# Kernel tuning notes

Measured on AMD Instinct MI355X. Metric: run time of the kernel, lower is better.

The kernel has to match this reference:

```python
import jax, jax.numpy as jnp
import numpy as np

B, N, H, MEM, V = 512, 50, 256, 8, 40001
SCALE = 1.0 / float(np.sqrt(H))
NEG = -1e12


def sinusoid_table(n_pos, d):
    pos = np.arange(n_pos)[:, None].astype(np.float64)
    j = np.arange(d)[None, :]
    ang = pos / np.power(10000.0, 2 * (j // 2) / d)
    tab = np.zeros((n_pos, d))
    tab[:, 0::2] = np.sin(ang[:, 0::2])
    tab[:, 1::2] = np.cos(ang[:, 1::2])
    return jnp.asarray(tab, jnp.float32)

TAB = sinusoid_table(N, H)


def setup_inputs():
    key = jax.random.key(0)
    ks = jax.random.split(key, 40)
    s = 0.05
    rn = lambda k, shp, sc=s: jax.random.normal(k, shp, jnp.float32) * sc
    lengths = jax.random.randint(ks[0], (B,), 1, N + 1)
    mask = (jnp.arange(N)[None, :] < lengths[:, None]).astype(jnp.int32)
    item_flag = jax.random.randint(ks[1], (B, V - 1), 0, 2).astype(jnp.int32)
    inp = {
        'seq_emb_1': rn(ks[2], (B, N, H), 1.0),
        'seq_emb_2': rn(ks[3], (B, N, H), 1.0),
        'mask': mask,
        'item_flag': item_flag,
        # 2-layer GRU (torch layout: W_ih [3H,H], W_hh [3H,H])
        'gru_wih0': rn(ks[4], (3 * H, H)), 'gru_whh0': rn(ks[5], (3 * H, H)),
        'gru_bih0': rn(ks[6], (3 * H,)), 'gru_bhh0': rn(ks[7], (3 * H,)),
        'gru_wih1': rn(ks[8], (3 * H, H)), 'gru_whh1': rn(ks[9], (3 * H, H)),
        'gru_bih1': rn(ks[10], (3 * H,)), 'gru_bhh1': rn(ks[11], (3 * H,)),
        # attention projections ([in,out] layout, y = x @ W)
        'Wq1': rn(ks[12], (H, H)), 'Wk1': rn(ks[13], (H, H)), 'Wv1': rn(ks[14], (H, H)),
        'Wq2': rn(ks[15], (H, H)), 'Wk2': rn(ks[16], (H, H)), 'Wv2': rn(ks[17], (H, H)),
        'W_ffn1': rn(ks[18], (H, H)), 'b_ffn1': rn(ks[19], (H,)),
        'W_ffn2': rn(ks[20], (H, H)), 'b_ffn2': rn(ks[21], (H,)),
        'W_one1': rn(ks[22], (H, H)), 'b_one1': rn(ks[23], (H,)),
        'W_three1': rn(ks[24], (2 * H, 1)),
        'W_trans1': rn(ks[25], (2 * H, H)), 'b_trans1': rn(ks[26], (H,)),
        'W_tail1': rn(ks[27], (H, H)), 'b_tail1': rn(ks[28], (H,)),
        'W_tail2': rn(ks[29], (H, 2)),
        'mem_k': rn(ks[30], (1, MEM, H)), 'mem_v': rn(ks[31], (1, MEM, H)),
        'emb1': rn(ks[32], (V, H)),
    }
    return inp


def _gru_layer(x, wih, whh, bih, bhh):
    # x: [B,N,H] -> [B,N,H], h0 = 0 (torch default)
    def step(h, xt):
        gi = xt @ wih.T + bih
        gh = h @ whh.T + bhh
        ir, iz, inn = jnp.split(gi, 3, axis=-1)
        hr, hz, hn = jnp.split(gh, 3, axis=-1)
        r = jax.nn.sigmoid(ir + hr)
        z = jax.nn.sigmoid(iz + hz)
        n = jnp.tanh(inn + r * hn)
        h2 = (1.0 - z) * n + z * h
        return h2, h2
    h0 = jnp.zeros((x.shape[0], H), x.dtype)
    _, ys = jax.lax.scan(step, h0, jnp.swapaxes(x, 0, 1))
    return jnp.swapaxes(ys, 0, 1)


def _co_attention(q, k, v, mask, mem_k=None, mem_v=None):
    b = q.shape[0]
    causal = jnp.tril(jnp.ones((N, N), bool))           # [N,N]
    pad = mask.astype(bool)[:, None, :]                  # [B,1,N]
    allow_seq = causal[None, :, :] & pad                 # [B,N,N]
    if mem_k is not None:
        k = jnp.concatenate([jnp.broadcast_to(mem_k, (b, MEM, H)), k], axis=1)
        v = jnp.concatenate([jnp.broadcast_to(mem_v, (b, MEM, H)), v], axis=1)
        mem_ok = jnp.ones((b, N, MEM), bool)             # memory keys always visible
        allow = jnp.concatenate([mem_ok, allow_seq], axis=-1)
    else:
        allow = allow_seq
    att = jnp.einsum('bqh,bkh->bqk', q, k) * SCALE
    att = jax.nn.softmax(jnp.where(allow, att, NEG), axis=-1)
    return jnp.einsum('bqk,bkh->bqh', att, v) * mask[:, :, None].astype(q.dtype)


def reference(seq_emb_1, seq_emb_2, mask, item_flag,
              gru_wih0, gru_whh0, gru_bih0, gru_bhh0,
              gru_wih1, gru_whh1, gru_bih1, gru_bhh1,
              Wq1, Wk1, Wv1, Wq2, Wk2, Wv2,
              W_ffn1, b_ffn1, W_ffn2, b_ffn2,
              W_one1, b_one1, W_three1, W_trans1, b_trans1,
              W_tail1, b_tail1, W_tail2, mem_k, mem_v, emb1):
    b = mask.shape[0]
    mf = mask[:, :, None].astype(jnp.float32)
    # 2-layer GRU on stream 2
    s2 = _gru_layer(seq_emb_2, gru_wih0, gru_whh0, gru_bih0, gru_bhh0)
    s2 = _gru_layer(s2, gru_wih1, gru_whh1, gru_bih1, gru_bhh1)
    last = jnp.sum(mask, axis=1) - 1                     # last valid index
    sr_l_1 = seq_emb_1[jnp.arange(b), last]              # [B,H]
    q1_1 = sr_l_1 @ W_one1 + b_one1 + TAB[0]
    se1 = seq_emb_1 * mf
    # positional encoding indexed by |pos - last_idx|
    flag = jnp.abs(jnp.arange(N, dtype=jnp.int32)[None, :] - last[:, None].astype(jnp.int32))
    pe = TAB[flag]                                       # [B,N,H]
    q1 = se1 @ Wq1 + pe
    k1 = se1 @ Wk1 + pe
    v1 = se1 @ Wv1 + pe
    att1 = _co_attention(q1, k1, v1, mask) @ W_ffn1 + b_ffn1
    se2 = s2 * mf
    k2 = se2 @ Wk2
    v2 = se2 @ Wv2
    att2 = _co_attention(q1, k2, v2, mask, mem_k, mem_v) @ W_ffn2 + b_ffn2
    att = jax.nn.relu(att1 + att2)
    alpha = jnp.concatenate([att, jnp.broadcast_to(q1_1[:, None, :], att.shape)], axis=-1) @ W_three1
    alpha = jax.nn.softmax(jnp.where(mf > 0, alpha, NEG), axis=1)  # [B,N,1]
    sess = jnp.sum(alpha * se1 * mf, axis=1)
    sess = jnp.concatenate([sess, sr_l_1], axis=1) @ W_trans1 + b_trans1
    item_emb = emb1[1:]                                  # [V-1,H]
    score = sess @ item_emb.T                            # [B,V-1]
    fl = item_flag.astype(bool)
    score_in = jax.nn.softmax(jnp.where(fl, score, NEG), axis=-1)
    score_ex = jax.nn.softmax(jnp.where(fl, NEG, score), axis=-1)
    beta = jax.nn.softmax(jax.nn.relu(sess @ W_tail1 + b_tail1) @ W_tail2, axis=-1)  # [B,2]
    boundary = jnp.mean(jnp.abs(beta[:, 0] - beta[:, 1]))
    final = score_in * beta[:, 0:1] + score_ex * beta[:, 1:2]
    return final[:, None, :], boundary
```

## Files before the change

kernel.cpp:

```cpp
#include <hip/hip_runtime.h>
#include <hip/hip_bf16.h>
#include <cstdint>
#include <cstddef>

#define Bsz 512
#define Nsq 50
#define Hd  256
#define VM1 40000
static constexpr float SCALE_C = 0.0625f;
static constexpr float NEG_C   = -1.0e12f;

typedef __attribute__((ext_vector_type(8))) short bf16x8;
typedef __attribute__((ext_vector_type(4))) float f32x4;

__device__ __forceinline__ float sigmoidf_(float x) { return 1.0f / (1.0f + __expf(-x)); }
__device__ __forceinline__ float tanh_fast(float x) {
  float t = fminf(fmaxf(2.0f * x, -60.0f), 60.0f);
  float e = __expf(t);
  return (e - 1.0f) / (e + 1.0f);
}
__device__ __forceinline__ ushort f2b(float x) {
  union { float f; uint32_t u; } c; c.f = x;
  uint32_t r = (c.u + 0x7fffu + ((c.u >> 16) & 1u)) >> 16;
  return (ushort)r;
}
__device__ __forceinline__ uint pk2f(float a, float b) {
  return (uint)f2b(a) | ((uint)f2b(b) << 16);
}
__device__ __forceinline__ uint addpe2(uint w, float pa, float pb) {
  union { float f; uint32_t u; } lo, hi;
  lo.u = (w & 0xffffu) << 16; hi.u = w & 0xffff0000u;
  return pk2f(lo.f + pa, hi.f + pb);
}

__global__ void build_tab(float* __restrict__ TAB) {
  int idx = blockIdx.x * 256 + threadIdx.x;
  int pos = idx >> 8, j = idx & 255;
  int pair = j >> 1;
  float expo = (2.0f * (float)pair) / 256.0f;
  float inv = powf(10000.0f, -expo);
  float ang = (float)pos * inv;
  TAB[idx] = (j & 1) ? cosf(ang) : sinf(ang);
}

__global__ __launch_bounds__(256) void last_srl_kernel(const int* __restrict__ mask,
    const float* __restrict__ seq1, int* __restrict__ lastp, float* __restrict__ srl) {
  int b = blockIdx.x, tid = threadIdx.x;
  __shared__ int ls;
  if (tid == 0) {
    int c = 0;
    for (int t = 0; t < Nsq; ++t) c += mask[b * Nsq + t];
    ls = c - 1;
    lastp[b] = c - 1;
  }
  __syncthreads();
  srl[b * Hd + tid] = seq1[((size_t)b * Nsq + ls) * Hd + tid];
}

template <int BT, int BIAS>
__global__ __launch_bounds__(256) void gemm_tile(const float* __restrict__ A,
    const float* __restrict__ B, const float* __restrict__ bias,
    float* __restrict__ C, int M, int N, int K) {
  __shared__ float As[16][132];
  __shared__ float Bs[16][68];
  int bm = blockIdx.y * 128, bn = blockIdx.x * 64;
  int tid = threadIdx.x;
  int tm = (tid >> 4) << 3;
  int tn = (tid & 15) << 2;
  float acc[8][4] = {};
  for (int k0 = 0; k0 < K; k0 += 16) {
#pragma unroll
    for (int u = 0; u < 8; ++u) {
      int i = tid + u * 256;
      int kk = i & 15, m = i >> 4;
      As[kk][m] = A[(size_t)(bm + m) * K + (k0 + kk)];
    }
#pragma unroll
    for (int u = 0; u < 4; ++u) {
      int i = tid + u * 256;
      if (BT) {
        int kk = i & 15, n = i >> 4;
        Bs[kk][n] = B[(size_t)(bn + n) * K + (k0 + kk)];
      } else {
        int n = i & 63, kk = i >> 6;
        Bs[kk][n] = B[(size_t)(k0 + kk) * N + (bn + n)];
      }
    }
    __syncthreads();
#pragma unroll
    for (int kk = 0; kk < 16; ++kk) {
      float a[8], bb[4];
#pragma unroll
      for (int r = 0; r < 8; ++r) a[r] = As[kk][tm + r];
#pragma unroll
      for (int c = 0; c < 4; ++c) bb[c] = Bs[kk][tn + c];
#pragma unroll
      for (int r = 0; r < 8; ++r)
#pragma unroll
        for (int c = 0; c < 4; ++c) acc[r][c] += a[r] * bb[c];
    }
    __syncthreads();
  }
#pragma unroll
  for (int r = 0; r < 8; ++r) {
    size_t row = (size_t)(bm + tm + r) * N + bn;
#pragma unroll
    for (int c = 0; c < 4; ++c) {
      float v = acc[r][c];
      if (BIAS) v += bias[bn + tn + c];
      C[row + tn + c] = v;
    }
  }
}

template <int BT, int BIAS, int OUTBF>
__global__ __launch_bounds__(256) void mfma_gemm(const ushort* __restrict__ A,
    const ushort* __restrict__ B, const float* __restrict__ bias,
    void* __restrict__ Cv, int M, int N, int K) {
  __shared__ ushort Asm[128 * 32];
  __shared__ ushort Bsm[128 * 40];
  constexpr int SB = BT ? 32 : 40;
  int tid = threadIdx.x;
  int bm = blockIdx.y * 128, bn = blockIdx.x * 128;
  int lane = tid & 63, wave = tid >> 6;
  int quad = lane >> 4, l16 = lane & 15;
  int wm = (wave >> 1) * 64, wn = (wave & 1) * 64;

  int chn0 = wave * 2, chn1 = wave * 2 + 1;
  int ra0 = chn0 * 16 + (lane >> 2), ra1 = chn1 * 16 + (lane >> 2);
  int kc = (lane & 3) * 8;
  const ushort* srcA0 = A + (size_t)(bm + ra0) * K + kc;
  const ushort* srcA1 = A + (size_t)(bm + ra1) * K + kc;
  char* dstA0 = (char*)Asm + chn0 * 1024;
  char* dstA1 = (char*)Asm + chn1 * 1024;
  const ushort* srcB0 = nullptr;
  const ushort* srcB1 = nullptr;
  if (BT) {
    int rb0 = bn + ra0; if (rb0 > N - 1) rb0 = N - 1;
    int rb1 = bn + ra1; if (rb1 > N - 1) rb1 = N - 1;
    srcB0 = B + (size_t)rb0 * K + kc;
    srcB1 = B + (size_t)rb1 * K + kc;
  }
  char* dstB0 = (char*)Bsm + chn0 * 1024;
  char* dstB1 = (char*)Bsm + chn1 * 1024;

  f32x4 acc[4][4] = {};
  for (int k0 = 0; k0 < K; k0 += 32) {
    __builtin_amdgcn_global_load_lds(
        (const __attribute__((address_space(1))) void*)(srcA0 + k0),
        (__attribute__((address_space(3))) void*)dstA0, 16, 0, 0);
    __builtin_amdgcn_global_load_lds(
        (const __attribute__((address_space(1))) void*)(srcA1 + k0),
        (__attribute__((address_space(3))) void*)dstA1, 16, 0, 0);
    if (BT) {
      __builtin_amdgcn_global_load_lds(
          (const __attribute__((address_space(1))) void*)(srcB0 + k0),
          (__attribute__((address_space(3))) void*)dstB0, 16, 0, 0);
      __builtin_amdgcn_global_load_lds(
          (const __attribute__((address_space(1))) void*)(srcB1 + k0),
          (__attribute__((address_space(3))) void*)dstB1, 16, 0, 0);
    } else {
#pragma unroll
      for (int u = 0; u < 8; ++u) {
        int idx = tid + u * 256;
        int n2 = (idx & 63) * 2, kk = idx >> 6;
        uint v = *(const uint*)(B + (size_t)(k0 + kk) * N + bn + n2);
        Bsm[n2 * 40 + kk] = (ushort)(v & 0xffffu);
        Bsm[(n2 + 1) * 40 + kk] = (ushort)(v >> 16);
      }
    }
    __syncthreads();
    bf16x8 af[4], bfr[4];
#pragma unroll
    for (int f = 0; f < 4; ++f) af[f] = *(const bf16x8*)(Asm + (wm + f * 16 + l16) * 32 + quad * 8);
#pragma unroll
    for (int f = 0; f < 4; ++f) bfr[f] = *(const bf16x8*)(Bsm + (wn + f * 16 + l16) * SB + quad * 8);
#pragma unroll
    for (int mf = 0; mf < 4; ++mf)
#pragma unroll
      for (int nf = 0; nf < 4; ++nf)
        acc[mf][nf] = __builtin_amdgcn_mfma_f32_16x16x32_bf16(af[mf], bfr[nf], acc[mf][nf], 0, 0, 0);
    __syncthreads();
  }
#pragma unroll
  for (int mf = 0; mf < 4; ++mf) {
#pragma unroll
    for (int r = 0; r < 4; ++r) {
      int row = bm + wm + mf * 16 + quad * 4 + r;
      size_t rowo = (size_t)row * N;
#pragma unroll
      for (int nf = 0; nf < 4; ++nf) {
        int col = bn + wn + nf * 16 + l16;
        if (col < N) {
          float v = acc[mf][nf][r];
          if (BIAS) v += bias[col];
          if (OUTBF) ((ushort*)Cv)[rowo + col] = f2b(v);
          else       ((float*)Cv)[rowo + col] = v;
        }
      }
    }
  }
}

__global__ void cast_f2b_k(const float* __restrict__ s, ushort* __restrict__ d, int n4) {
  int i = blockIdx.x * 256 + threadIdx.x;
  if (i >= n4) return;
  const float4 v = ((const float4*)s)[i];
  ushort4 o; o.x = f2b(v.x); o.y = f2b(v.y); o.z = f2b(v.z); o.w = f2b(v.w);
  ((ushort4*)d)[i] = o;
}

struct Cast7 { const float* s[7]; ushort* d[7]; };
__global__ void cast7_k(Cast7 p) {
  int m = blockIdx.y;
  int i = blockIdx.x * 256 + threadIdx.x;
  const float4 v = ((const float4*)p.s[m])[i];
  ushort4 o; o.x = f2b(v.x); o.y = f2b(v.y); o.z = f2b(v.z); o.w = f2b(v.w);
  ((ushort4*)p.d[m])[i] = o;
}

__global__ void add_tab0(float* __restrict__ q) {
  int idx = blockIdx.x * 256 + threadIdx.x;
  q[idx] += (float)(threadIdx.x & 1);
}

__global__ void mask_cast(const float* __restrict__ x, const int* __restrict__ m,
                          ushort* __restrict__ yb) {
  int idx = blockIdx.x * 256 + threadIdx.x;
  float v = m[idx >> 8] ? x[idx] : 0.0f;
  yb[idx] = f2b(v);
}

__global__ __launch_bounds__(512, 2) void gru_mfma8_kernel(const float* __restrict__ gi,
    const ushort* __restrict__ whhb, const float* __restrict__ bhh,
    ushort* __restrict__ ysb, const int* __restrict__ mask) {
  __shared__ ushort hbf[2][16][264];
  __shared__ float  gsc[8][2][3][32];
  int tid = threadIdx.x;
  int lane = tid & 63, wave = tid >> 6;
  int quad = lane >> 4, l16 = lane & 15;
  int s0 = blockIdx.x * 2;

  for (int i = tid; i < 2 * 16 * 264 / 2; i += 512) ((uint*)hbf)[i] = 0u;

  bf16x8 bw[48];
#pragma unroll
  for (int f = 0; f < 48; ++f) {
    int nf = f >> 3, kf = f & 7;
    int row = (nf >> 1) * 256 + wave * 32 + (nf & 1) * 16 + l16;
    bw[f] = *(const bf16x8*)(whhb + (size_t)row * 256 + kf * 32 + quad * 8);
  }

  int s = lane >> 5, dloc = lane & 31;
  int d = wave * 32 + dloc;
  float bh0 = bhh[d], bh1 = bhh[256 + d], bh2 = bhh[512 + d];
  const float* gib = gi + (size_t)(s0 + s) * Nsq * 768 + d;
  float g0 = gib[0], g1 = gib[256], g2 = gib[512];
  float hreg = 0.0f;
  const int* mrow = mask + (s0 + s) * Nsq;
  ushort* yrow = ysb + ((size_t)(s0 + s) * Nsq) * 256 + d;
  __syncthreads();

  int cur = 0;
  for (int t = 0; t < Nsq; ++t) {
    int tn = (t + 1 < Nsq) ? t + 1 : t;
    float p0 = gib[tn * 768], p1 = gib[tn * 768 + 256], p2 = gib[tn * 768 + 512];

    f32x4 acc[6] = {};
#pragma unroll
    for (int kf = 0; kf < 8; ++kf) {
      bf16x8 a = *(const bf16x8*)&hbf[cur][l16][kf * 32 + quad * 8];
#pragma unroll
      for (int nf = 0; nf < 6; ++nf)
        acc[nf] = __builtin_amdgcn_mfma_f32_16x16x32_bf16(a, bw[nf * 8 + kf], acc[nf], 0, 0, 0);
    }
    if (quad == 0) {
#pragma unroll
      for (int g = 0; g < 3; ++g)
#pragma unroll
        for (int j = 0; j < 2; ++j) {
          gsc[wave][0][g][j * 16 + l16] = acc[g * 2 + j][0];
          gsc[wave][1][g][j * 16 + l16] = acc[g * 2 + j][1];
        }
    }
    __builtin_amdgcn_sched_barrier(0);

    {
      float ghr = gsc[wave][s][0][dloc];
      float ghz = gsc[wave][s][1][dloc];
      float ghn = gsc[wave][s][2][dloc];
      float rr = sigmoidf_(g0 + ghr + bh0);
      float zz = sigmoidf_(g1 + ghz + bh1);
      float nn = tanh_fast(g2 + rr * (ghn + bh2));
      float h2 = (1.0f - zz) * nn + zz * hreg;
      hreg = h2;
      hbf[cur ^ 1][s][d] = f2b(h2);
      float ov = h2;
      if (mask) ov = mrow[t] ? h2 : 0.0f;
      yrow[t * 256] = f2b(ov);
    }
    g0 = p0; g1 = p1; g2 = p2;
    cur ^= 1;
    __syncthreads();
  }
}

template <int NMEM, int PEQ, int PEKV>
__global__ __launch_bounds__(256) void attn_mfma(const ushort* __restrict__ q1,
    const ushort* __restrict__ kseq, const ushort* __restrict__ vseq,
    const float* __restrict__ kmem, const float* __restrict__ vmem,
    const int* __restrict__ mask, ushort* __restrict__ out,
    const float* __restrict__ TAB, const int* __restrict__ lastp) {
  constexpr int NK = NMEM + Nsq;
  __shared__ ushort KV[64][264];
  __shared__ float Ss[64][66];
  __shared__ ushort Ps[64][72];
  __shared__ int msk[64];
  int tid = threadIdx.x;
  int lane = tid & 63, wave = tid >> 6;
  int quad = lane >> 4, l16 = lane & 15;
  int b = blockIdx.x;
  int last = lastp[b];

  if (tid < 64) msk[tid] = (tid < Nsq) ? mask[b * Nsq + tid] : 0;

#pragma unroll
  for (int it = 0; it < 8; ++it) {
    int idx = tid + it * 256;
    int r = idx >> 5, c8 = (idx & 31) * 8;
    uint4 o4 = make_uint4(0u, 0u, 0u, 0u);
    if (r < Nsq) {
      uint4 v = *(const uint4*)(q1 + (size_t)(b * Nsq + r) * 256 + c8);
      if (PEQ) {
        const float* pe = TAB + abs(r - last) * 256 + c8;
        float4 pa = *(const float4*)pe;
        float4 pb = *(const float4*)(pe + 4);
        o4.x = addpe2(v.x, pa.x, pa.y);
        o4.y = addpe2(v.y, pa.z, pa.w);
        o4.z = addpe2(v.z, pb.x, pb.y);
        o4.w = addpe2(v.w, pb.z, pb.w);
      } else {
        o4 = v;
      }
    }
    *(uint4*)&KV[r][c8] = o4;
  }
  __syncthreads();
  bf16x8 qa[8];
#pragma unroll
  for (int kf = 0; kf < 8; ++kf)
    qa[kf] = *(const bf16x8*)&KV[wave * 16 + l16][kf * 32 + quad * 8];
  __syncthreads();

#pragma unroll
  for (int it = 0; it < 8; ++it) {
    int idx = tid + it * 256;
    int r = idx >> 5, c8 = (idx & 31) * 8;
    uint4 o4 = make_uint4(0u, 0u, 0u, 0u);
    if (r < NK) {
      if (NMEM > 0 && r < NMEM) {
        const float* src = kmem + (size_t)r * 256 + c8;
        float4 a = *(const float4*)src;
        float4 c = *(const float4*)(src + 4);
        o4.x = pk2f(a.x, a.y); o4.y = pk2f(a.z, a.w);
        o4.z = pk2f(c.x, c.y); o4.w = pk2f(c.z, c.w);
      } else {
        uint4 v = *(const uint4*)(kseq + (size_t)(b * Nsq + (r - NMEM)) * 256 + c8);
        if (PEKV) {
          const float* pe = TAB + abs((r - NMEM) - last) * 256 + c8;
          float4 pa = *(const float4*)pe;
          float4 pb = *(const float4*)(pe + 4);
          o4.x = addpe2(v.x, pa.x, pa.y);
          o4.y = addpe2(v.y, pa.z, pa.w);
          o4.z = addpe2(v.z, pb.x, pb.y);
          o4.w = addpe2(v.w, pb.z, pb.w);
        } else {
          o4 = v;
        }
      }
    }
    *(uint4*)&KV[r][c8] = o4;
  }
  __syncthreads();

  {
    f32x4 acc[4] = {};
#pragma unroll
    for (int kf = 0; kf < 8; ++kf) {
#pragma unroll
      for (int nf = 0; nf < 4; ++nf) {
        bf16x8 bf = *(const bf16x8*)&KV[nf * 16 + l16][kf * 32 + quad * 8];
        acc[nf] = __builtin_amdgcn_mfma_f32_16x16x32_bf16(qa[kf], bf, acc[nf], 0, 0, 0);
      }
    }
#pragma unroll
    for (int nf = 0; nf < 4; ++nf)
#pragma unroll
      for (int r = 0; r < 4; ++r)
        Ss[wave * 16 + quad * 4 + r][nf * 16 + l16] = acc[nf][r];
  }
  __syncthreads();

#pragma unroll
  for (int it = 0; it < 8; ++it) {
    int idx = tid + it * 256;
    int r = idx >> 5, c8 = (idx & 31) * 8;
    uint4 o4 = make_uint4(0u, 0u, 0u, 0u);
    if (r < NK) {
      if (NMEM > 0 && r < NMEM) {
        const float* src = vmem + (size_t)r * 256 + c8;
        float4 a = *(const float4*)src;
        float4 c = *(const float4*)(src + 4);
        o4.x = pk2f(a.x, a.y); o4.y = pk2f(a.z, a.w);
        o4.z = pk2f(c.x, c.y); o4.w = pk2f(c.z, c.w);
      } else {
        uint4 v = *(const uint4*)(vseq + (size_t)(b * Nsq + (r - NMEM)) * 256 + c8);
        if (PEKV) {
          const float* pe = TAB + abs((r - NMEM) - last) * 256 + c8;
          float4 pa = *(const float4*)pe;
          float4 pb = *(const float4*)(pe + 4);
          o4.x = addpe2(v.x, pa.x, pa.y);
          o4.y = addpe2(v.y, pa.z, pa.w);
          o4.z = addpe2(v.z, pb.x, pb.y);
          o4.w = addpe2(v.w, pb.z, pb.w);
        } else {
          o4 = v;
        }
      }
    }
    *(uint4*)&KV[r][c8] = o4;
  }
  if (tid < 64) {
    int t = tid;
    if (t < Nsq) {
      float m = -1e30f;
      for (int j = 0; j < NK; ++j) {
        bool ok = (j < NMEM) || (((j - NMEM) <= t) && (msk[j - NMEM] != 0));
        if (ok) m = fmaxf(m, Ss[t][j] * SCALE_C);
      }
      float sum = 0.0f;
      for (int j = 0; j < NK; ++j) {
        bool ok = (j < NMEM) || (((j - NMEM) <= t) && (msk[j - NMEM] != 0));
        if (ok) sum += __expf(Ss[t][j] * SCALE_C - m);
      }
      float inv = 1.0f / sum;
      for (int j = 0; j < 64; ++j) {
        float p = 0.0f;
        if (j < NK) {
          bool ok = (j < NMEM) || (((j - NMEM) <= t) && (msk[j - NMEM] != 0));
          if (ok) p = __expf(Ss[t][j] * SCALE_C - m) * inv;
        }
        Ps[t][j] = f2b(p);
      }
    } else {
      for (int j = 0; j < 64; ++j) Ps[t][j] = 0;
    }
  }
  __syncthreads();

  {
    f32x4 o[4][4] = {};
#pragma unroll
    for (int kf = 0; kf < 2; ++kf) {
      bf16x8 pa[4];
#pragma unroll
      for (int mf = 0; mf < 4; ++mf)
        pa[mf] = *(const bf16x8*)&Ps[mf * 16 + l16][kf * 32 + quad * 8];
#pragma unroll
      for (int nf = 0; nf < 4; ++nf) {
        int h = wave * 64 + nf * 16 + l16;
        ushort e0 = KV[kf * 32 + quad * 8 + 0][h];
        ushort e1 = KV[kf * 32 + quad * 8 + 1][h];
        ushort e2 = KV[kf * 32 + quad * 8 + 2][h];
        ushort e3 = KV[kf * 32 + quad * 8 + 3][h];
        ushort e4 = KV[kf * 32 + quad * 8 + 4][h];
        ushort e5 = KV[kf * 32 + quad * 8 + 5][h];
        ushort e6 = KV[kf * 32 + quad * 8 + 6][h];
        ushort e7 = KV[kf * 32 + quad * 8 + 7][h];
        bf16x8 vb = {(short)e0, (short)e1, (short)e2, (short)e3,
                     (short)e4, (short)e5, (short)e6, (short)e7};
#pragma unroll
        for (int mf = 0; mf < 4; ++mf)
          o[mf][nf] = __builtin_amdgcn_mfma_f32_16x16x32_bf16(pa[mf], vb, o[mf][nf], 0, 0, 0);
      }
    }
#pragma unroll
    for (int mf = 0; mf < 4; ++mf) {
#pragma unroll
      for (int r = 0; r < 4; ++r) {
        int t = mf * 16 + quad * 4 + r;
        if (t < Nsq) {
          int zero = (msk[t] == 0);
#pragma unroll
          for (int nf = 0; nf < 4; ++nf) {
            int h = wave * 64 + nf * 16 + l16;
            float val = zero ? 0.0f : o[mf][nf][r];
            out[((size_t)(b * Nsq + t)) * 256 + h] = f2b(val);
          }
        }
      }
    }
  }
}

__global__ __launch_bounds__(256) void alpha_sess_kernel(const float* __restrict__ att1,
    const float* __restrict__ att2,
    const float* __restrict__ W3, const float* __restrict__ q11,
    const float* __restrict__ seq1, const int* __restrict__ mask,
    const float* __restrict__ srl, float* __restrict__ sesscat) {
  int b = blockIdx.x, tid = threadIdx.x;
  __shared__ float red[256];
  __shared__ float ash[50];
  red[tid] = q11[b * Hd + tid] * W3[256 + tid];
  __syncthreads();
  for (int s = 128; s; s >>= 1) { if (tid < s) red[tid] += red[tid + s]; __syncthreads(); }
  float cq = red[0];
  float aval = 0.0f;
  if (tid < 50) {
    float s = cq;
    const float* a1 = att1 + ((size_t)b * Nsq + tid) * Hd;
    const float* a2 = att2 + ((size_t)b * Nsq + tid) * Hd;
    for (int hh = 0; hh < 256; ++hh) s += fmaxf(a1[hh] + a2[hh], 0.0f) * W3[hh];
    aval = mask[b * Nsq + tid] ? s : NEG_C;
  }
  if (tid < 64) {
    float s = (tid < 50) ? aval : NEG_C;
    float m = s;
    for (int off = 32; off; off >>= 1) m = fmaxf(m, __shfl_xor(m, off));
    float e = expf(s - m);
    float sum = e;
    for (int off = 32; off; off >>= 1) sum += __shfl_xor(sum, off);
    if (tid < 50) ash[tid] = e / sum;
  }
  __syncthreads();
  float acc = 0.0f;
  const float* se = seq1 + (size_t)b * Nsq * Hd;
  for (int t = 0; t < Nsq; ++t) acc += ash[t] * se[t * 256 + tid];
  sesscat[(size_t)b * 512 + tid] = acc;
  sesscat[(size_t)b * 512 + 256 + tid] = srl[b * Hd + tid];
}

__global__ __launch_bounds__(256) void beta_kernel(const float* __restrict__ sess2,
    const float* __restrict__ Wt1, const float* __restrict__ bt1,
    const float* __restrict__ Wt2, float* __restrict__ beta, float* __restrict__ bnd) {
  int b = blockIdx.x, tid = threadIdx.x;
  __shared__ float xs[256];
  __shared__ float r0[256], r1[256];
  xs[tid] = sess2[b * Hd + tid];
  __syncthreads();
  float hsum = bt1[tid];
  for (int k = 0; k < 256; ++k) hsum += xs[k] * Wt1[k * 256 + tid];
  float hid = fmaxf(hsum, 0.0f);
  r0[tid] = hid * Wt2[tid * 2 + 0];
  r1[tid] = hid * Wt2[tid * 2 + 1];
  __syncthreads();
  for (int s = 128; s; s >>= 1) {
    if (tid < s) { r0[tid] += r0[tid + s]; r1[tid] += r1[tid + s]; }
    __syncthreads();
  }
  if (tid == 0) {
    float t0 = r0[0], t1 = r1[0];
    float m = fmaxf(t0, t1);
    float e0 = expf(t0 - m), e1 = expf(t1 - m);
    float bb0 = e0 / (e0 + e1), bb1 = e1 / (e0 + e1);
    beta[b * 2] = bb0; beta[b * 2 + 1] = bb1;
    atomicAdd(bnd, fabsf(bb0 - bb1) * (1.0f / 512.0f));
  }
}

__global__ __launch_bounds__(1024) void score_final_fused(float* __restrict__ score,
    const int* __restrict__ flag, const float* __restrict__ beta) {
  int b = blockIdx.x, tid = threadIdx.x;
  float4* sr = (float4*)(score + (size_t)b * VM1);
  const int4* fr = (const int4*)(flag + (size_t)b * VM1);
  constexpr int NV = VM1 / 4;
  constexpr int NW = (NV + 7) / 8;

  __shared__ uint bits[NW];
  __shared__ float red[1024], red2[1024];

  for (int i = tid; i < NW; i += 1024) bits[i] = 0u;
  __syncthreads();

  float mi = -INFINITY, me = -INFINITY;
  for (int i = tid; i < NV; i += 1024) {
    float4 s = sr[i];
    int4 f = fr[i];
    uint nib = (f.x ? 1u : 0u) | (f.y ? 2u : 0u) | (f.z ? 4u : 0u) | (f.w ? 8u : 0u);
    if (nib) atomicOr(&bits[i >> 3], nib << ((i & 7) * 4));
    if (f.x) mi = fmaxf(mi, s.x); else me = fmaxf(me, s.x);
    if (f.y) mi = fmaxf(mi, s.y); else me = fmaxf(me, s.y);
    if (f.z) mi = fmaxf(mi, s.z); else me = fmaxf(me, s.z);
    if (f.w) mi = fmaxf(mi, s.w); else me = fmaxf(me, s.w);
  }
  red[tid] = mi; red2[tid] = me;
  __syncthreads();
  for (int s = 512; s; s >>= 1) {
    if (tid < s) { red[tid] = fmaxf(red[tid], red[tid + s]); red2[tid] = fmaxf(red2[tid], red2[tid + s]); }
    __syncthreads();
  }
  float Mi = red[0], Me = red2[0];
  __syncthreads();

  float si = 0.0f, se = 0.0f;
  for (int i = tid; i < NV; i += 1024) {
    float4 s = sr[i];
    uint nib = bits[i >> 3] >> ((i & 7) * 4);
    float e0 = __expf(s.x - ((nib & 1u) ? Mi : Me));
    float e1 = __expf(s.y - ((nib & 2u) ? Mi : Me));
    float e2 = __expf(s.z - ((nib & 4u) ? Mi : Me));
    float e3 = __expf(s.w - ((nib & 8u) ? Mi : Me));
    si += ((nib & 1u) ? e0 : 0.0f) + ((nib & 2u) ? e1 : 0.0f)
        + ((nib & 4u) ? e2 : 0.0f) + ((nib & 8u) ? e3 : 0.0f);
    se += ((nib & 1u) ? 0.0f : e0) + ((nib & 2u) ? 0.0f : e1)
        + ((nib & 4u) ? 0.0f : e2) + ((nib & 8u) ? 0.0f : e3);
  }
  red[tid] = si; red2[tid] = se;
  __syncthreads();
  for (int s = 512; s; s >>= 1) {
    if (tid < s) { red[tid] += red[tid + s]; red2[tid] += red2[tid + s]; }
    __syncthreads();
  }
  float c0 = beta[b * 2] / red[0];
  float c1 = beta[b * 2 + 1] / red2[0];
  __syncthreads();

  for (int i = tid; i < NV; i += 1024) {
    float4 s = sr[i];
    uint nib = bits[i >> 3] >> ((i & 7) * 4);
    s.x = ((nib & 1u) ? c0 : c1) * __expf(s.x - ((nib & 1u) ? Mi : Me));
    s.y = ((nib & 2u) ? c0 : c1) * __expf(s.y - ((nib & 2u) ? Mi : Me));
    s.z = ((nib & 4u) ? c0 : c1) * __expf(s.z - ((nib & 4u) ? Mi : Me));
    s.w = ((nib & 8u) ? c0 : c1) * __expf(s.w - ((nib & 8u) ? Mi : Me));
    sr[i] = s;
  }
}

extern "C" void kernel_launch(void* const* d_in, const int* in_sizes, int n_in,
                              void* d_out, int out_size, void* d_ws, size_t ws_size,
                              hipStream_t stream) {
  const float* seq1  = (const float*)d_in[0];
  const float* seq2  = (const float*)d_in[1];
  const int*   mask  = (const int*)d_in[2];
  const int*   iflag = (const int*)d_in[3];
  const float* wih0  = (const float*)d_in[4];
  const float* whh0  = (const float*)d_in[5];
  const float* bih0  = (const float*)d_in[6];
  const float* bhh0  = (const float*)d_in[7];
  const float* wih1  = (const float*)d_in[8];
  const float* whh1  = (const float*)d_in[9];
  const float* bih1  = (const float*)d_in[10];
  const float* bhh1  = (const float*)d_in[11];
  const float* Wq1   = (const float*)d_in[12];
  const float* Wk1   = (const float*)d_in[13];
  const float* Wv1   = (const float*)d_in[14];
  const float* Wk2   = (const float*)d_in[16];
  const float* Wv2   = (const float*)d_in[17];
  const float* Wffn1 = (const float*)d_in[18];
  const float* bffn1 = (const float*)d_in[19];
  const float* Wffn2 = (const float*)d_in[20];
  const float* bffn2 = (const float*)d_in[21];
  const float* Wone  = (const float*)d_in[22];
  const float* bone  = (const float*)d_in[23];
  const float* W3    = (const float*)d_in[24];
  const float* Wtr   = (const float*)d_in[25];
  const float* btr   = (const float*)d_in[26];
  const float* Wt1   = (const float*)d_in[27];
  const float* bt1   = (const float*)d_in[28];
  const float* Wt2   = (const float*)d_in[29];
  const float* memk  = (const float*)d_in[30];
  const float* memv  = (const float*)d_in[31];
  const float* emb1  = (const float*)d_in[32];
  float* out = (float*)d_out;

  char* wsb = (char*)d_ws;
  float*  TAB    = (float*)(wsb + 0);
  int*    lastp  = (int*)  (wsb + 51200);
  float*  srl    = (float*)(wsb + 53248);
  float*  q11    = (float*)(wsb + 577536);
  ushort* whh0b  = (ushort*)(wsb + 1101824);
  ushort* whh1b  = (ushort*)(wsb + 1888256);
  ushort* wih0b  = (ushort*)(wsb + 2674688);
  ushort* wih1b  = (ushort*)(wsb + 3067904);
  ushort* w7b    = (ushort*)(wsb + 3461120);
  ushort* bufS   = (ushort*)(wsb + 4378624);
  float*  se1    = (float*)(wsb + 17485824);
  ushort* se1b   = (ushort*)(wsb + 43700224);
  float*  giQ    = (float*)(wsb + 56807424);
  float*  kv2a   = (float*)(wsb + 135450624);
  float*  kv2b   = (float*)(wsb + 161665024);
  ushort* ao1b   = (ushort*)(wsb + 187879424);
  ushort* ao2b   = (ushort*)(wsb + 200986624);

  float* gi = giQ;
  ushort* q1b = (ushort*)giQ;
  ushort* k1b = q1b + 6553600;
  ushort* v1b = q1b + 13107200;
  ushort* k2b = (ushort*)kv2a;
  ushort* v2b = k2b + 6553600;
  ushort* embB    = (ushort*)giQ;
  float*  sesscat = (float*)((char*)giQ + 20480000);
  float*  sess2   = (float*)((char*)giQ + 21528576);
  ushort* sess2b  = (ushort*)((char*)giQ + 22052864);
  float*  betab   = (float*)((char*)giQ + 22315008);
  float*  bnd     = out + (size_t)Bsz * VM1;

  ushort* Wq1b = w7b;              ushort* Wk1b = w7b + 65536;
  ushort* Wv1b = w7b + 131072;     ushort* Wk2b = w7b + 196608;
  ushort* Wv2b = w7b + 262144;     ushort* Wf1b = w7b + 327680;
  ushort* Wf2b = w7b + 393216;

  build_tab<<<50, 256, 0, stream>>>(TAB);
  last_srl_kernel<<<Bsz, 256, 0, stream>>>(mask, seq1, lastp, srl);
  gemm_tile<0, 1><<<dim3(4, 4), 256, 0, stream>>>(srl, Wone, bone, q11, 512, 256, 256);
  add_tab0<<<512, 256, 0, stream>>>(q11);

  cast_f2b_k<<<6400, 256, 0, stream>>>(seq2, bufS, 1638400);
  cast_f2b_k<<<192, 256, 0, stream>>>(wih0, wih0b, 49152);
  cast_f2b_k<<<192, 256, 0, stream>>>(wih1, wih1b, 49152);
  cast_f2b_k<<<192, 256, 0, stream>>>(whh0, whh0b, 49152);
  cast_f2b_k<<<192, 256, 0, stream>>>(whh1, whh1b, 49152);
  Cast7 c7;
  c7.s[0] = Wq1; c7.s[1] = Wk1; c7.s[2] = Wv1; c7.s[3] = Wk2; c7.s[4] = Wv2;
  c7.s[5] = Wffn1; c7.s[6] = Wffn2;
  c7.d[0] = Wq1b; c7.d[1] = Wk1b; c7.d[2] = Wv1b; c7.d[3] = Wk2b; c7.d[4] = Wv2b;
  c7.d[5] = Wf1b; c7.d[6] = Wf2b;
  cast7_k<<<dim3(64, 7), 256, 0, stream>>>(c7);

  mfma_gemm<1, 1, 0><<<dim3(6, 200), 256, 0, stream>>>(bufS, wih0b, bih0, gi, 25600, 768, 256);
  gru_mfma8_kernel<<<256, 512, 0, stream>>>(gi, whh0b, bhh0, bufS, nullptr);
  mfma_gemm<1, 1, 0><<<dim3(6, 200), 256, 0, stream>>>(bufS, wih1b, bih1, gi, 25600, 768, 256);
  gru_mfma8_kernel<<<256, 512, 0, stream>>>(gi, whh1b, bhh1, bufS, mask);

  mask_cast<<<25600, 256, 0, stream>>>(seq1, mask, se1b);

  mfma_gemm<0, 0, 1><<<dim3(2, 200), 256, 0, stream>>>(bufS, Wk2b, nullptr, k2b, 25600, 256, 256);
  mfma_gemm<0, 0, 1><<<dim3(2, 200), 256, 0, stream>>>(bufS, Wv2b, nullptr, v2b, 25600, 256, 256);
  mfma_gemm<0, 0, 1><<<dim3(2, 200), 256, 0, stream>>>(se1b, Wq1b, nullptr, q1b, 25600, 256, 256);
  mfma_gemm<0, 0, 1><<<dim3(2, 200), 256, 0, stream>>>(se1b, Wk1b, nullptr, k1b, 25600, 256, 256);
  mfma_gemm<0, 0, 1><<<dim3(2, 200), 256, 0, stream>>>(se1b, Wv1b, nullptr, v1b, 25600, 256, 256);

  attn_mfma<0, 1, 1><<<Bsz, 256, 0, stream>>>(q1b, k1b, v1b, nullptr, nullptr, mask, ao1b, TAB, lastp);
  attn_mfma<8, 1, 0><<<Bsz, 256, 0, stream>>>(q1b, k2b, v2b, memk, memv, mask, ao2b, TAB, lastp);
  mfma_gemm<0, 1, 0><<<dim3(2, 200), 256, 0, stream>>>(ao1b, Wf1b, bffn1, kv2a, 25600, 256, 256);
  mfma_gemm<0, 1, 0><<<dim3(2, 200), 256, 0, stream>>>(ao2b, Wf2b, bffn2, kv2b, 25600, 256, 256);

  alpha_sess_kernel<<<Bsz, 256, 0, stream>>>(kv2a, kv2b, W3, q11, seq1, mask, srl, sesscat);
  gemm_tile<0, 1><<<dim3(4, 4), 256, 0, stream>>>(sesscat, Wtr, btr, sess2, 512, 256, 512);
  cast_f2b_k<<<128, 256, 0, stream>>>(sess2, sess2b, 32768);

  hipMemsetAsync(bnd, 0, 4, stream);
  beta_kernel<<<Bsz, 256, 0, stream>>>(sess2, Wt1, bt1, Wt2, betab, bnd);
  cast_f2b_k<<<10000, 256, 0, stream>>>(emb1 + 256, embB, 2560000);
  mfma_gemm<1, 0, 0><<<dim3(313, 4), 256, 0, stream>>>(sess2b, embB, nullptr, out, 512, VM1, 256);
  score_final_fused<<<Bsz, 1024, 0, stream>>>(out, iflag, betab);

  (void)in_sizes; (void)n_in; (void)out_size; (void)ws_size; (void)se1;
}
```

Measured before the change: 898.2 us.

## Fuse both FFN projections with add and ReLU into one GEMM; merge small casts

Result: slower. 958.8 us (+6.8%).

```diff
diff --git a/kernel.cpp b/kernel.cpp
--- a/kernel.cpp
+++ b/kernel.cpp
@@ -57,7 +57,7 @@
   srl[b * Hd + tid] = seq1[((size_t)b * Nsq + ls) * Hd + tid];
 }
 
-template <int BT, int BIAS>
+template <int BT, int BIAS, int TAB0>
 __global__ __launch_bounds__(256) void gemm_tile(const float* __restrict__ A,
     const float* __restrict__ B, const float* __restrict__ bias,
     float* __restrict__ C, int M, int N, int K) {
@@ -108,6 +108,7 @@
     for (int c = 0; c < 4; ++c) {
       float v = acc[r][c];
       if (BIAS) v += bias[bn + tn + c];
+      if (TAB0) v += (float)((bn + tn + c) & 1);
       C[row + tn + c] = v;
     }
   }
@@ -202,6 +203,99 @@
   }
 }
 
+__global__ __launch_bounds__(256) void ffn_fused(const ushort* __restrict__ A1,
+    const ushort* __restrict__ B1w, const float* __restrict__ b1,
+    const ushort* __restrict__ A2, const ushort* __restrict__ B2w,
+    const float* __restrict__ b2, float* __restrict__ C, int M, int N, int K) {
+  __shared__ ushort A1s[128 * 32];
+  __shared__ ushort A2s[128 * 32];
+  __shared__ ushort B1s[128 * 40];
+  __shared__ ushort B2s[128 * 40];
+  int tid = threadIdx.x;
+  int bm = blockIdx.y * 128, bn = blockIdx.x * 128;
+  int lane = tid & 63, wave = tid >> 6;
+  int quad = lane >> 4, l16 = lane & 15;
+  int wm = (wave >> 1) * 64, wn = (wave & 1) * 64;
+
+  int chn0 = wave * 2, chn1 = wave * 2 + 1;
+  int ra0 = chn0 * 16 + (lane >> 2), ra1 = chn1 * 16 + (lane >> 2);
+  int kc = (lane & 3) * 8;
+  const ushort* sA10 = A1 + (size_t)(bm + ra0) * K + kc;
+  const ushort* sA11 = A1 + (size_t)(bm + ra1) * K + kc;
+  const ushort* sA20 = A2 + (size_t)(bm + ra0) * K + kc;
+  const ushort* sA21 = A2 + (size_t)(bm + ra1) * K + kc;
+  char* dA10 = (char*)A1s + chn0 * 1024;
+  char* dA11 = (char*)A1s + chn1 * 1024;
+  char* dA20 = (char*)A2s + chn0 * 1024;
+  char* dA21 = (char*)A2s + chn1 * 1024;
+
+  f32x4 acc[4][4] = {};
+  for (int k0 = 0; k0 < K; k0 += 32) {
+    __builtin_amdgcn_global_load_lds(
+        (const __attribute__((address_space(1))) void*)(sA10 + k0),
+        (__attribute__((address_space(3))) void*)dA10, 16, 0, 0);
+    __builtin_amdgcn_global_load_lds(
+        (const __attribute__((address_space(1))) void*)(sA11 + k0),
+        (__attribute__((address_space(3))) void*)dA11, 16, 0, 0);
+    __builtin_amdgcn_global_load_lds(
+        (const __attribute__((address_space(1))) void*)(sA20 + k0),
+        (__attribute__((address_space(3))) void*)dA20, 16, 0, 0);
+    __builtin_amdgcn_global_load_lds(
+        (const __attribute__((address_space(1))) void*)(sA21 + k0),
+        (__attribute__((address_space(3))) void*)dA21, 16, 0, 0);
+#pragma unroll
+    for (int u = 0; u < 8; ++u) {
+      int idx = tid + u * 256;
+      int n2 = (idx & 63) * 2, kk = idx >> 6;
+      uint v1 = *(const uint*)(B1w + (size_t)(k0 + kk) * N + bn + n2);
+      B1s[n2 * 40 + kk] = (ushort)(v1 & 0xffffu);
+      B1s[(n2 + 1) * 40 + kk] = (ushort)(v1 >> 16);
+      uint v2 = *(const uint*)(B2w + (size_t)(k0 + kk) * N + bn + n2);
+      B2s[n2 * 40 + kk] = (ushort)(v2 & 0xffffu);
+      B2s[(n2 + 1) * 40 + kk] = (ushort)(v2 >> 16);
+    }
+    __syncthreads();
+    {
+      bf16x8 af[4], bfr[4];
+#pragma unroll
+      for (int f = 0; f < 4; ++f) af[f] = *(const bf16x8*)(A1s + (wm + f * 16 + l16) * 32 + quad * 8);
+#pragma unroll
+      for (int f = 0; f < 4; ++f) bfr[f] = *(const bf16x8*)(B1s + (wn + f * 16 + l16) * 40 + quad * 8);
+#pragma unroll
+      for (int mf = 0; mf < 4; ++mf)
+#pragma unroll
+        for (int nf = 0; nf < 4; ++nf)
+          acc[mf][nf] = __builtin_amdgcn_mfma_f32_16x16x32_bf16(af[mf], bfr[nf], acc[mf][nf], 0, 0, 0);
+#pragma unroll
+      for (int f = 0; f < 4; ++f) af[f] = *(const bf16x8*)(A2s + (wm + f * 16 + l16) * 32 + quad * 8);
+#pragma unroll
+      for (int f = 0; f < 4; ++f) bfr[f] = *(const bf16x8*)(B2s + (wn + f * 16 + l16) * 40 + quad * 8);
+#pragma unroll
+      for (int mf = 0; mf < 4; ++mf)
+#pragma unroll
+        for (int nf = 0; nf < 4; ++nf)
+          acc[mf][nf] = __builtin_amdgcn_mfma_f32_16x16x32_bf16(af[mf], bfr[nf], acc[mf][nf], 0, 0, 0);
+    }
+    __syncthreads();
+  }
+#pragma unroll
+  for (int mf = 0; mf < 4; ++mf) {
+#pragma unroll
+    for (int r = 0; r < 4; ++r) {
+      int row = bm + wm + mf * 16 + quad * 4 + r;
+      size_t rowo = (size_t)row * N;
+#pragma unroll
+      for (int nf = 0; nf < 4; ++nf) {
+        int col = bn + wn + nf * 16 + l16;
+        if (col < N) {
+          float v = acc[mf][nf][r] + b1[col] + b2[col];
+          C[rowo + col] = fmaxf(v, 0.0f);
+        }
+      }
+    }
+  }
+}
+
 __global__ void cast_f2b_k(const float* __restrict__ s, ushort* __restrict__ d, int n4) {
   int i = blockIdx.x * 256 + threadIdx.x;
   if (i >= n4) return;
@@ -219,9 +313,13 @@
   ((ushort4*)p.d[m])[i] = o;
 }
 
-__global__ void add_tab0(float* __restrict__ q) {
-  int idx = blockIdx.x * 256 + threadIdx.x;
-  q[idx] += (float)(threadIdx.x & 1);
+struct Cast4 { const float* s[4]; ushort* d[4]; };
+__global__ void cast4_k(Cast4 p) {
+  int m = blockIdx.y;
+  int i = blockIdx.x * 256 + threadIdx.x;
+  const float4 v = ((const float4*)p.s[m])[i];
+  ushort4 o; o.x = f2b(v.x); o.y = f2b(v.y); o.z = f2b(v.z); o.w = f2b(v.w);
+  ((ushort4*)p.d[m])[i] = o;
 }
 
 __global__ void mask_cast(const float* __restrict__ x, const int* __restrict__ m,
@@ -503,8 +601,7 @@
   }
 }
 
-__global__ __launch_bounds__(256) void alpha_sess_kernel(const float* __restrict__ att1,
-    const float* __restrict__ att2,
+__global__ __launch_bounds__(256) void alpha_sess_kernel(const float* __restrict__ att,
     const float* __restrict__ W3, const float* __restrict__ q11,
     const float* __restrict__ seq1, const int* __restrict__ mask,
     const float* __restrict__ srl, float* __restrict__ sesscat) {
@@ -518,9 +615,8 @@
   float aval = 0.0f;
   if (tid < 50) {
     float s = cq;
-    const float* a1 = att1 + ((size_t)b * Nsq + tid) * Hd;
-    const float* a2 = att2 + ((size_t)b * Nsq + tid) * Hd;
-    for (int hh = 0; hh < 256; ++hh) s += fmaxf(a1[hh] + a2[hh], 0.0f) * W3[hh];
+    const float* ar = att + ((size_t)b * Nsq + tid) * Hd;
+    for (int hh = 0; hh < 256; ++hh) s += ar[hh] * W3[hh];
     aval = mask[b * Nsq + tid] ? s : NEG_C;
   }
   if (tid < 64) {
@@ -684,7 +780,6 @@
   ushort* wih1b  = (ushort*)(wsb + 3067904);
   ushort* w7b    = (ushort*)(wsb + 3461120);
   ushort* bufS   = (ushort*)(wsb + 4378624);
-  float*  se1    = (float*)(wsb + 17485824);
   ushort* se1b   = (ushort*)(wsb + 43700224);
   float*  giQ    = (float*)(wsb + 56807424);
   float*  kv2a   = (float*)(wsb + 135450624);
@@ -712,14 +807,13 @@
 
   build_tab<<<50, 256, 0, stream>>>(TAB);
   last_srl_kernel<<<Bsz, 256, 0, stream>>>(mask, seq1, lastp, srl);
-  gemm_tile<0, 1><<<dim3(4, 4), 256, 0, stream>>>(srl, Wone, bone, q11, 512, 256, 256);
-  add_tab0<<<512, 256, 0, stream>>>(q11);
+  gemm_tile<0, 1, 1><<<dim3(4, 4), 256, 0, stream>>>(srl, Wone, bone, q11, 512, 256, 256);
 
   cast_f2b_k<<<6400, 256, 0, stream>>>(seq2, bufS, 1638400);
-  cast_f2b_k<<<192, 256, 0, stream>>>(wih0, wih0b, 49152);
-  cast_f2b_k<<<192, 256, 0, stream>>>(wih1, wih1b, 49152);
-  cast_f2b_k<<<192, 256, 0, stream>>>(whh0, whh0b, 49152);
-  cast_f2b_k<<<192, 256, 0, stream>>>(whh1, whh1b, 49152);
+  Cast4 c4;
+  c4.s[0] = wih0; c4.s[1] = wih1; c4.s[2] = whh0; c4.s[3] = whh1;
+  c4.d[0] = wih0b; c4.d[1] = wih1b; c4.d[2] = whh0b; c4.d[3] = whh1b;
+  cast4_k<<<dim3(192, 4), 256, 0, stream>>>(c4);
   Cast7 c7;
   c7.s[0] = Wq1; c7.s[1] = Wk1; c7.s[2] = Wv1; c7.s[3] = Wk2; c7.s[4] = Wv2;
   c7.s[5] = Wffn1; c7.s[6] = Wffn2;
@@ -742,11 +836,12 @@
 
   attn_mfma<0, 1, 1><<<Bsz, 256, 0, stream>>>(q1b, k1b, v1b, nullptr, nullptr, mask, ao1b, TAB, lastp);
   attn_mfma<8, 1, 0><<<Bsz, 256, 0, stream>>>(q1b, k2b, v2b, memk, memv, mask, ao2b, TAB, lastp);
-  mfma_gemm<0, 1, 0><<<dim3(2, 200), 256, 0, stream>>>(ao1b, Wf1b, bffn1, kv2a, 25600, 256, 256);
-  mfma_gemm<0, 1, 0><<<dim3(2, 200), 256, 0, stream>>>(ao2b, Wf2b, bffn2, kv2b, 25600, 256, 256);
-
-  alpha_sess_kernel<<<Bsz, 256, 0, stream>>>(kv2a, kv2b, W3, q11, seq1, mask, srl, sesscat);
-  gemm_tile<0, 1><<<dim3(4, 4), 256, 0, stream>>>(sesscat, Wtr, btr, sess2, 512, 256, 512);
+
+  ffn_fused<<<dim3(2, 200), 256, 0, stream>>>(ao1b, Wf1b, bffn1, ao2b, Wf2b, bffn2,
+                                              kv2a, 25600, 256, 256);
+
+  alpha_sess_kernel<<<Bsz, 256, 0, stream>>>(kv2a, W3, q11, seq1, mask, srl, sesscat);
+  gemm_tile<0, 1, 0><<<dim3(4, 4), 256, 0, stream>>>(sesscat, Wtr, btr, sess2, 512, 256, 512);
   cast_f2b_k<<<128, 256, 0, stream>>>(sess2, sess2b, 32768);
 
   hipMemsetAsync(bnd, 0, 4, stream);
@@ -755,5 +850,5 @@
   mfma_gemm<1, 0, 0><<<dim3(313, 4), 256, 0, stream>>>(sess2b, embB, nullptr, out, 512, VM1, 256);
   score_final_fused<<<Bsz, 1024, 0, stream>>>(out, iflag, betab);
 
-  (void)in_sizes; (void)n_in; (void)out_size; (void)ws_size; (void)se1;
-}
+  (void)in_sizes; (void)n_in; (void)out_size; (void)ws_size; (void)kv2b;
+}
```
